# Kernel optimization log

Hardware: AMD Instinct MI355X
Metric: run time of the kernel (lower is better)

Reference implementation:

```python
import jax, jax.numpy as jnp
import numpy as np
from jax import lax

B, C, H, W = 4, 256, 64, 64
C8 = C // 8


def _conv1x1(x, w, b):
    # x: (B,C,H,W), w: (O,C) -> (B,O,H,W)
    return jnp.einsum('bchw,oc->bohw', x, w) + b[None, :, None, None]


def setup_inputs() -> dict:
    key = jax.random.key(0)
    ks = jax.random.split(key, 9)
    s1 = 1.0 / np.sqrt(C)          # fan-in scale for 1x1 convs
    sf = 1.0 / np.sqrt(2 * C * 9)  # fan-in scale for 3x3 conv
    return {
        'front_x':     jax.random.normal(ks[0], (B, C, H, W), jnp.float32),
        'cross_x':     jax.random.normal(ks[1], (B, C, H, W), jnp.float32),
        'front_x_hat': jax.random.normal(ks[2], (B, C, H, W), jnp.float32),
        'Wq': jax.random.normal(ks[3], (C8, C), jnp.float32) * s1,
        'bq': jnp.zeros((C8,), jnp.float32),
        'Wk': jax.random.normal(ks[4], (C8, C), jnp.float32) * s1,
        'bk': jnp.zeros((C8,), jnp.float32),
        'Wv': jax.random.normal(ks[5], (C, C), jnp.float32) * s1,
        'bv': jnp.zeros((C,), jnp.float32),
        'Wf': jax.random.normal(ks[6], (C, 2 * C, 3, 3), jnp.float32) * sf,
        'bf': jnp.zeros((C,), jnp.float32),
    }


def reference(front_x, cross_x, front_x_hat, Wq, bq, Wk, bk, Wv, bv, Wf, bf):
    b, c, h, w = front_x.shape
    hw = h * w
    # projections -> (B, C/8, HW)
    q = _conv1x1(cross_x, Wq, bq).reshape(b, -1, hw)
    k = _conv1x1(front_x, Wk, bk).reshape(b, -1, hw)
    # energy[b,i,j] = <key_i, query_j>  (B, HW, HW)
    energy = jnp.einsum('bci,bcj->bij', k, q)
    front_star = jnp.max(energy, axis=1)     # (B, HW) best key score per query
    front_arg = jnp.argmax(energy, axis=1)   # (B, HW) best key index per query
    # value projection and hard gather of best-matching value per position
    v = _conv1x1(front_x_hat, Wv, bv).reshape(b, c, hw)
    T = jnp.take_along_axis(v, front_arg[:, None, :], axis=2).reshape(b, c, h, w)
    S = front_star.reshape(b, 1, h, w)
    cat = jnp.concatenate([front_x, T], axis=1)  # (B, 2C, H, W)
    res = lax.conv_general_dilated(
        cat, Wf, window_strides=(1, 1), padding='SAME',
        dimension_numbers=('NCHW', 'OIHW', 'NCHW')) + bf[None, :, None, None]
    return front_x + res * S
```

## Files before the change

kernel.cpp:

```cpp
#include <hip/hip_runtime.h>

#define Bn 4
#define Cn 256
#define C8 32
#define Hn 64
#define Wn 64
#define HWn 4096
#define PADR 80
#define ROWS (HWn + 2 * PADR)
#define MARGIN 6e-3f

typedef __bf16 bf16x8 __attribute__((ext_vector_type(8)));
typedef float floatx4 __attribute__((ext_vector_type(4)));
typedef unsigned short u16x8 __attribute__((ext_vector_type(8)));

__device__ __forceinline__ unsigned short f2bf(float f) {
  union { float f; unsigned int u; } c; c.f = f;
  unsigned int u = c.u;
  return (unsigned short)((u + 0x7FFFu + ((u >> 16) & 1u)) >> 16);
}
__device__ __forceinline__ float bf2f(unsigned short h) {
  union { unsigned int u; float f; } c; c.u = ((unsigned int)h) << 16;
  return c.f;
}
__device__ __forceinline__ void gl_lds16(const void* g, void* l) {
  __builtin_amdgcn_global_load_lds(
      (__attribute__((address_space(1))) void*)(uintptr_t)g,
      (__attribute__((address_space(3))) void*)(uintptr_t)l, 16, 0, 0);
}

__global__ void prep_w(const float* __restrict__ Wq, const float* __restrict__ Wk,
                       const float* __restrict__ Wv, const float* __restrict__ Wf,
                       float* __restrict__ Wqf, float* __restrict__ Wkf,
                       unsigned short* __restrict__ Wvb, unsigned short* __restrict__ Wfb,
                       int* __restrict__ cnt) {
  size_t t = (size_t)blockIdx.x * 256 + threadIdx.x;
  if (t == 0) cnt[0] = 0;
  if (t < 8192) {
    int o = (int)(t / 256), c = (int)(t % 256);
    Wqf[(size_t)c * 32 + o] = Wq[t];
    Wkf[(size_t)c * 32 + o] = Wk[t];
  }
  if (t < 65536) Wvb[t] = f2bf(Wv[t]);
  if (t < (size_t)9 * 256 * 512) {
    int tap = (int)(t / (256 * 512));
    int rem = (int)(t % (256 * 512));
    int o = rem / 512, ci = rem % 512;
    Wfb[t] = f2bf(Wf[((size_t)o * 512 + ci) * 9 + tap]);
  }
}

__global__ __launch_bounds__(1024) void proj_qk(
    const float* __restrict__ cross_x, const float* __restrict__ front_x,
    const float* __restrict__ Wqf, const float* __restrict__ bq,
    const float* __restrict__ Wkf, const float* __restrict__ bk,
    float* __restrict__ qf, float* __restrict__ kf,
    unsigned short* __restrict__ qhi, unsigned short* __restrict__ qlo,
    unsigned short* __restrict__ khi, unsigned short* __restrict__ klo) {
  int tid = threadIdx.x;
  int lane = tid & 63, wv = tid >> 6;
  int slice = wv & 3;
  int chunk = wv >> 2;
  int j = blockIdx.x * 64 + lane;
  int b = blockIdx.y;
  int z = blockIdx.z;
  const float* x = (z == 0) ? cross_x : front_x;
  const float* Wg = (z == 0) ? Wqf : Wkf;
  const float* bd = (z == 0) ? bq : bk;
  float* outp = (z == 0) ? qf : kf;
  unsigned short* hip_ = (z == 0) ? qhi : khi;
  unsigned short* lop_ = (z == 0) ? qlo : klo;
  int o0 = slice * 8;
  int c0 = chunk * 64;

  __shared__ __align__(16) float Wl[8192];
  __shared__ float part[3 * 4 * 8 * 64];

  for (int u = tid; u < 8192; u += 1024) Wl[u] = Wg[u];
  __syncthreads();

  const float* xb = x + (size_t)b * Cn * HWn + j;
  floatx4 a0 = (floatx4)0.0f, a1 = (floatx4)0.0f;
#pragma unroll 16
  for (int c = c0; c < c0 + 64; ++c) {
    float xv = xb[(size_t)c * HWn];
    floatx4 wa = *reinterpret_cast<const floatx4*>(&Wl[c * 32 + o0]);
    floatx4 wb = *reinterpret_cast<const floatx4*>(&Wl[c * 32 + o0 + 4]);
    a0 += wa * xv;
    a1 += wb * xv;
  }
  if (chunk > 0) {
    float* dst = &part[(((chunk - 1) * 4 + slice) * 8) * 64];
#pragma unroll
    for (int o = 0; o < 4; ++o) { dst[o * 64 + lane] = a0[o]; dst[(o + 4) * 64 + lane] = a1[o]; }
  }
  __syncthreads();
  if (chunk != 0) return;
#pragma unroll
  for (int q = 0; q < 3; ++q) {
    const float* src = &part[((q * 4 + slice) * 8) * 64];
#pragma unroll
    for (int o = 0; o < 4; ++o) { a0[o] += src[o * 64 + lane]; a1[o] += src[(o + 4) * 64 + lane]; }
  }
  float acc[8];
#pragma unroll
  for (int o = 0; o < 4; ++o) { acc[o] = a0[o] + bd[o0 + o]; acc[o + 4] = a1[o] + bd[o0 + 4 + o]; }

  float* op = outp + ((size_t)b * HWn + j) * C8 + o0;
  u16x8 hv, lv;
#pragma unroll
  for (int o = 0; o < 8; ++o) {
    op[o] = acc[o];
    unsigned short h = f2bf(acc[o]);
    hv[o] = h;
    lv[o] = f2bf(acc[o] - bf2f(h));
  }
  *reinterpret_cast<u16x8*>(hip_ + ((size_t)b * HWn + j) * C8 + o0) = hv;
  *reinterpret_cast<u16x8*>(lop_ + ((size_t)b * HWn + j) * C8 + o0) = lv;
}

__global__ __launch_bounds__(1024) void energy_approx(
    const unsigned short* __restrict__ khi, const unsigned short* __restrict__ klo,
    const unsigned short* __restrict__ qhi, const unsigned short* __restrict__ qlo,
    float* __restrict__ star, int* __restrict__ argb,
    int* __restrict__ cnt, int* __restrict__ list) {
  int b = blockIdx.y;
  int j0 = blockIdx.x * 32;
  int tid = threadIdx.x;
  int lane = tid & 63, wv = tid >> 6;
  int lm = lane & 15, lq = lane >> 4;

  __shared__ float bv1S[16][32];
  __shared__ int   bi1S[16][32];
  __shared__ float bv2S[16][32];

  bf16x8 qh[2], ql[2];
#pragma unroll
  for (int s = 0; s < 2; ++s) {
    int j = j0 + s * 16 + lm;
    qh[s] = *reinterpret_cast<const bf16x8*>(qhi + ((size_t)b * HWn + j) * 32 + lq * 8);
    ql[s] = *reinterpret_cast<const bf16x8*>(qlo + ((size_t)b * HWn + j) * 32 + lq * 8);
  }
  const unsigned short* kh_base = khi + (size_t)b * HWn * 32 + lq * 8;
  const unsigned short* kl_base = klo + (size_t)b * HWn * 32 + lq * 8;

  float b1[2], b2[2];
#pragma unroll
  for (int s = 0; s < 2; ++s) { b1[s] = -3.0e38f; b2[s] = -3.0e38f; }

  int ibase = wv * 256;
#pragma unroll 4
  for (int it = 0; it < 16; ++it) {
    int i0 = ibase + it * 16;
    bf16x8 ah = *reinterpret_cast<const bf16x8*>(kh_base + (size_t)(i0 + lm) * 32);
    bf16x8 al = *reinterpret_cast<const bf16x8*>(kl_base + (size_t)(i0 + lm) * 32);
#pragma unroll
    for (int s = 0; s < 2; ++s) {
      floatx4 acc = (floatx4)0.0f;
      acc = __builtin_amdgcn_mfma_f32_16x16x32_bf16(ah, qh[s], acc, 0, 0, 0);
      acc = __builtin_amdgcn_mfma_f32_16x16x32_bf16(ah, ql[s], acc, 0, 0, 0);
      acc = __builtin_amdgcn_mfma_f32_16x16x32_bf16(al, qh[s], acc, 0, 0, 0);
#pragma unroll
      for (int r = 0; r < 4; ++r) {
        unsigned code = (unsigned)(it * 4 + r);
        union { float f; unsigned u; } cv; cv.f = acc[r];
        cv.u = (cv.u & ~63u) | code;
        float vp = cv.f;
        b2[s] = __builtin_amdgcn_fmed3f(vp, b1[s], b2[s]);
        b1[s] = fmaxf(b1[s], vp);
      }
    }
  }
  int i1[2];
#pragma unroll
  for (int s = 0; s < 2; ++s) {
    union { float f; unsigned u; } cv; cv.f = b1[s];
    unsigned code = cv.u & 63u;
    i1[s] = ibase + (int)(code >> 2) * 16 + lq * 4 + (int)(code & 3u);
  }
#pragma unroll
  for (int s = 0; s < 2; ++s) {
#pragma unroll
    for (int m = 16; m <= 32; m <<= 1) {
      float ob1 = __shfl_xor(b1[s], m, 64);
      int oi1 = __shfl_xor(i1[s], m, 64);
      float ob2 = __shfl_xor(b2[s], m, 64);
      float c2;
      if (ob1 > b1[s] || (ob1 == b1[s] && oi1 < i1[s])) {
        c2 = fmaxf(b1[s], ob2);
        b1[s] = ob1; i1[s] = oi1;
      } else {
        c2 = fmaxf(ob1, b2[s]);
      }
      b2[s] = c2;
    }
    if (lq == 0) {
      bv1S[wv][s * 16 + lm] = b1[s];
      bi1S[wv][s * 16 + lm] = i1[s];
      bv2S[wv][s * 16 + lm] = b2[s];
    }
  }
  __syncthreads();
  if (tid < 32) {
    float B1 = bv1S[0][tid];
    int I1 = bi1S[0][tid];
    float B2 = bv2S[0][tid];
#pragma unroll
    for (int w = 1; w < 16; ++w) {
      float v1 = bv1S[w][tid];
      int ii = bi1S[w][tid];
      float v2 = bv2S[w][tid];
      if (v1 > B1) { B2 = fmaxf(B1, v2); B1 = v1; I1 = ii; }
      else B2 = fmaxf(B2, v1);
    }
    size_t o = (size_t)b * HWn + j0 + tid;
    union { float f; unsigned u; } cs; cs.f = B1;
    cs.u &= ~63u;
    star[o] = cs.f;
    argb[o] = I1;
    if (B1 - B2 < MARGIN) {
      int slot = atomicAdd(cnt, 1);
      list[slot] = (b << 12) | (j0 + (int)tid);
    }
  }
}

__global__ __launch_bounds__(256) void recheck(
    const float* __restrict__ qf, const float* __restrict__ kf,
    const int* __restrict__ cnt, const int* __restrict__ list,
    float* __restrict__ star, int* __restrict__ argb) {
  __shared__ double bvS[4];
  __shared__ int biS[4];
  int n = cnt[0];
  int tid = threadIdx.x;
  int lane = tid & 63, wv = tid >> 6;
  for (int idx = blockIdx.x; idx < n; idx += gridDim.x) {
    int e = list[idx];
    int b = e >> 12, j = e & 4095;
    const float* qp = qf + ((size_t)b * HWn + j) * 32;
    double qj[32];
#pragma unroll
    for (int o = 0; o < 32; ++o) qj[o] = (double)qp[o];
    double best = -1.0e300;
    int bi = 1 << 30;
    for (int i = tid; i < HWn; i += 256) {
      const float* kp = kf + ((size_t)b * HWn + i) * 32;
      double s = 0.0;
#pragma unroll
      for (int o = 0; o < 32; ++o) s += (double)kp[o] * qj[o];
      if (s > best) { best = s; bi = i; }
    }
#pragma unroll
    for (int m = 1; m < 64; m <<= 1) {
      double ob = __shfl_xor(best, m, 64);
      int oi = __shfl_xor(bi, m, 64);
      if (ob > best || (ob == best && oi < bi)) { best = ob; bi = oi; }
    }
    if (lane == 0) { bvS[wv] = best; biS[wv] = bi; }
    __syncthreads();
    if (tid == 0) {
#pragma unroll
      for (int w = 1; w < 4; ++w) {
        if (bvS[w] > best || (bvS[w] == best && biS[w] < bi)) {
          best = bvS[w]; bi = biS[w];
        }
      }
      star[(size_t)b * HWn + j] = (float)best;
      argb[(size_t)b * HWn + j] = bi;
    }
    __syncthreads();
  }
}

__global__ __launch_bounds__(256) void cat_fx(
    const float* __restrict__ fx, const float* __restrict__ fxh,
    unsigned short* __restrict__ catC, unsigned short* __restrict__ xht) {
  int j0 = blockIdx.x * 64;
  int ci0 = blockIdx.y * 64;
  int b = blockIdx.z >> 1;
  int which = blockIdx.z & 1;
  int tid = threadIdx.x;
  __shared__ unsigned short tile[64][66];

  const float* src = (which == 0) ? fx : fxh;
#pragma unroll
  for (int u = tid; u < 1024; u += 256) {
    int cl = u >> 4, h4 = (u & 15) * 4;
    floatx4 v = *reinterpret_cast<const floatx4*>(
        &src[((size_t)(b * Cn + ci0 + cl)) * HWn + j0 + h4]);
#pragma unroll
    for (int k = 0; k < 4; ++k) tile[cl][h4 + k] = f2bf(v[k]);
  }
  __syncthreads();
#pragma unroll
  for (int u = tid; u < 512; u += 256) {
    int oct = u & 7, hw_l = u >> 3;
    u16x8 val;
#pragma unroll
    for (int k = 0; k < 8; ++k) val[k] = tile[oct * 8 + k][hw_l];
    if (which == 0)
      *reinterpret_cast<u16x8*>(
          &catC[((size_t)b * ROWS + PADR + j0 + hw_l) * 512 + ci0 + oct * 8]) = val;
    else
      *reinterpret_cast<u16x8*>(
          &xht[((size_t)b * HWn + j0 + hw_l) * 256 + ci0 + oct * 8]) = val;
  }
}

__global__ __launch_bounds__(256) void proj_v_mfma(
    const unsigned short* __restrict__ xht, const unsigned short* __restrict__ Wvb,
    const float* __restrict__ bv, unsigned short* __restrict__ vbf) {
  int m0 = blockIdx.x * 128;
  int o0 = blockIdx.y * 128;
  int b = blockIdx.z;
  int tid = threadIdx.x;
  int lane = tid & 63, wv = tid >> 6;
  int wm = wv >> 1, wn = wv & 1;
  int lm = lane & 15, lq = lane >> 4;

  union SMu {
    struct { unsigned short A[2][128 * 32]; unsigned short B[2][128 * 32]; } st;
    unsigned short TS[128 * 136];
  };
  __shared__ __align__(16) SMu sm;

  floatx4 acc[4][4];
#pragma unroll
  for (int im = 0; im < 4; ++im)
#pragma unroll
    for (int in = 0; in < 4; ++in) acc[im][in] = (floatx4)0.0f;

  const int srow = lane >> 2;
  const int soff = (((lane & 3) ^ ((lane >> 3) & 3)) * 8);
  const int sa = (lq ^ ((lm >> 1) & 3)) * 8;
  const unsigned short* ag = Wvb + (size_t)o0 * 256;
  const unsigned short* bg = xht + ((size_t)b * HWn + m0) * 256;

  auto STAGE = [&](int buf, int kc) {
#pragma unroll
    for (int i = 0; i < 2; ++i) {
      int r0 = wv * 32 + i * 16;
      gl_lds16(ag + ((size_t)(r0 + srow)) * 256 + kc + soff, &sm.st.A[buf][r0 * 32]);
      gl_lds16(bg + ((size_t)(r0 + srow)) * 256 + kc + soff, &sm.st.B[buf][r0 * 32]);
    }
  };
  auto COMPUTE = [&](int buf) {
    bf16x8 afr[4];
#pragma unroll
    for (int im = 0; im < 4; ++im)
      afr[im] = *reinterpret_cast<const bf16x8*>(
          &sm.st.A[buf][(wm * 64 + im * 16 + lm) * 32 + sa]);
#pragma unroll
    for (int in = 0; in < 4; ++in) {
      bf16x8 bfr = *reinterpret_cast<const bf16x8*>(
          &sm.st.B[buf][(wn * 64 + in * 16 + lm) * 32 + sa]);
#pragma unroll
      for (int im = 0; im < 4; ++im)
        acc[im][in] = __builtin_amdgcn_mfma_f32_16x16x32_bf16(
            afr[im], bfr, acc[im][in], 0, 0, 0);
    }
  };

  STAGE(0, 0);
#pragma unroll 2
  for (int st = 0; st < 8; ++st) {
    __builtin_amdgcn_s_barrier();
    if (st < 7) {
      STAGE((st + 1) & 1, (st + 1) * 32);
      asm volatile("s_waitcnt vmcnt(4)" ::: "memory");
    } else {
      asm volatile("s_waitcnt vmcnt(0)" ::: "memory");
    }
    __builtin_amdgcn_s_barrier();
    __builtin_amdgcn_sched_barrier(0);
    COMPUTE(st & 1);
  }
  __builtin_amdgcn_s_barrier();

#pragma unroll
  for (int in = 0; in < 4; ++in) {
    int pl = wn * 64 + in * 16 + lm;
#pragma unroll
    for (int im = 0; im < 4; ++im) {
#pragma unroll
      for (int r = 0; r < 4; ++r) {
        int ol = wm * 64 + im * 16 + lq * 4 + r;
        sm.TS[pl * 136 + ol] = f2bf(acc[im][in][r] + bv[o0 + ol]);
      }
    }
  }
  __syncthreads();
  for (int idx = tid; idx < 128 * 16; idx += 256) {
    int p = idx >> 4, ch = idx & 15;
    u16x8 val = *reinterpret_cast<const u16x8*>(&sm.TS[p * 136 + ch * 8]);
    *reinterpret_cast<u16x8*>(
        &vbf[((size_t)b * HWn + m0 + p) * 256 + o0 + ch * 8]) = val;
  }
}

__global__ __launch_bounds__(256) void gather_cat(
    const unsigned short* __restrict__ vbf, const int* __restrict__ argb,
    unsigned short* __restrict__ catC) {
  int b = blockIdx.y;
  int tid = threadIdx.x;
  if (blockIdx.x == 16) {
    for (int u = tid; u < 2 * PADR * 512; u += 256) {
      int r = u >> 9;
      int rr = (r < PADR) ? r : (HWn + r);
      catC[((size_t)b * ROWS + rr) * 512 + (u & 511)] = 0;
    }
    return;
  }
  __shared__ int ajS[256];
  int j0 = blockIdx.x * 256;
  ajS[tid] = argb[(size_t)b * HWn + j0 + tid];
  __syncthreads();
#pragma unroll 4
  for (int u = tid; u < 256 * 32; u += 256) {
    int pl = u >> 5, ch = u & 31;
    int aj = ajS[pl];
    u16x8 val = *reinterpret_cast<const u16x8*>(
        &vbf[((size_t)b * HWn + aj) * 256 + ch * 8]);
    *reinterpret_cast<u16x8*>(
        &catC[((size_t)b * ROWS + PADR + j0 + pl) * 512 + 256 + ch * 8]) = val;
  }
}

__global__ __launch_bounds__(256) void conv_mfma(
    const unsigned short* __restrict__ catC, const unsigned short* __restrict__ Wfb,
    unsigned short* __restrict__ Pg) {
  int m0 = blockIdx.x * 128;
  int o0 = blockIdx.y * 128;
  int bz = blockIdx.z;
  int b = bz / 3, g = bz % 3;
  int dy = g - 1;
  int tid = threadIdx.x;
  int lane = tid & 63;
  int wv = tid >> 6;
  int wm = wv >> 1, wn = wv & 1;
  int lm = lane & 15, lq = lane >> 4;
  const bool lane_first = (lm == 0);
  const bool lane_last = (lm == 15);

  __shared__ __align__(16) unsigned short AS[2][3 * 128 * 32];
  __shared__ __align__(16) unsigned short BS[2][144 * 32];

  floatx4 acc[4][4];
#pragma unroll
  for (int im = 0; im < 4; ++im)
#pragma unroll
    for (int in = 0; in < 4; ++in) acc[im][in] = (floatx4)0.0f;

  const int srow = lane >> 2;
  const int soff = (((lane & 3) ^ ((lane >> 3) & 3)) * 8);
  const int sa = (lq ^ ((lm >> 1) & 3)) * 8;
  const unsigned short* bg =
      catC + ((size_t)b * ROWS + PADR + m0 + dy * 64 - 1) * 512;
  const unsigned short* ag = Wfb + ((size_t)(g * 3) * 256 + o0) * 512;

  auto STAGE = [&](unsigned short* ASb, unsigned short* BSb, int kc) {
    if (wv < 3) {
      const unsigned short* at = ag + (size_t)wv * 256 * 512;
#pragma unroll
      for (int s = 0; s < 8; ++s)
        gl_lds16(at + ((size_t)(s * 16 + srow)) * 512 + kc + soff,
                 &ASb[(wv * 128 + s * 16) * 32]);
    } else {
#pragma unroll
      for (int s = 0; s < 9; ++s)
        gl_lds16(bg + ((size_t)(s * 16 + srow)) * 512 + kc + soff,
                 &BSb[(s * 16) * 32]);
    }
  };
  auto COMPUTE = [&](const unsigned short* ASb, const unsigned short* BSb) {
#pragma unroll
    for (int t = 0; t < 3; ++t) {
      bf16x8 afr[4];
#pragma unroll
      for (int im = 0; im < 4; ++im)
        afr[im] = *reinterpret_cast<const bf16x8*>(
            &ASb[(t * 128 + wm * 64 + im * 16 + lm) * 32 + sa]);
#pragma unroll
      for (int in = 0; in < 4; ++in) {
        int u = wn * 64 + in * 16 + lm + t;
        int sb = (lq ^ ((u >> 1) & 3)) * 8;
        u16x8 braw = *reinterpret_cast<const u16x8*>(&BSb[u * 32 + sb]);
        if ((t == 0 && in == 0 && lane_first) ||
            (t == 2 && in == 3 && lane_last))
          braw = (u16x8)(unsigned short)0;
        union { u16x8 u8; bf16x8 h; } cvt; cvt.u8 = braw;
#pragma unroll
        for (int im = 0; im < 4; ++im)
          acc[im][in] = __builtin_amdgcn_mfma_f32_16x16x32_bf16(
              afr[im], cvt.h, acc[im][in], 0, 0, 0);
      }
    }
  };

  STAGE(AS[0], BS[0], 0);
  __syncthreads();
  for (int kci = 0; kci < 16; kci += 2) {
    if (kci < 15) STAGE(AS[1], BS[1], (kci + 1) * 32);
    COMPUTE(AS[0], BS[0]);
    __syncthreads();
    if (kci < 14) STAGE(AS[0], BS[0], (kci + 2) * 32);
    COMPUTE(AS[1], BS[1]);
    __syncthreads();
  }

  unsigned short* P = Pg + ((size_t)(g * Bn + b) * Cn) * HWn;
#pragma unroll
  for (int in = 0; in < 4; ++in) {
    int p = m0 + wn * 64 + in * 16 + lm;
#pragma unroll
    for (int im = 0; im < 4; ++im) {
      int ob = o0 + wm * 64 + im * 16 + lq * 4;
#pragma unroll
      for (int r = 0; r < 4; ++r)
        P[(size_t)(ob + r) * HWn + p] = f2bf(acc[im][in][r]);
    }
  }
}

__global__ __launch_bounds__(256) void combine(
    const unsigned short* __restrict__ Pg, const float* __restrict__ fx,
    const float* __restrict__ bf, const float* __restrict__ star,
    float* __restrict__ out) {
  size_t e = ((size_t)blockIdx.x * 256 + threadIdx.x) * 8;
  int p = (int)(e & 4095);
  int bo = (int)(e >> 12);
  int o = bo & 255, b = bo >> 8;
  const size_t gs = (size_t)Bn * Cn * HWn;
  u16x8 q0 = *reinterpret_cast<const u16x8*>(Pg + e);
  u16x8 q1 = *reinterpret_cast<const u16x8*>(Pg + gs + e);
  u16x8 q2 = *reinterpret_cast<const u16x8*>(Pg + 2 * gs + e);
  float bias = bf[o];
  const float* sp = star + (size_t)b * HWn + p;
  const float* fp = fx + e;
  float* op = out + e;
#pragma unroll
  for (int h = 0; h < 2; ++h) {
    floatx4 s = *reinterpret_cast<const floatx4*>(sp + h * 4);
    floatx4 f = *reinterpret_cast<const floatx4*>(fp + h * 4);
    floatx4 r;
#pragma unroll
    for (int i = 0; i < 4; ++i) {
      int k = h * 4 + i;
      float a = bf2f(q0[k]) + bf2f(q1[k]) + bf2f(q2[k]);
      r[i] = f[i] + (a + bias) * s[i];
    }
    *reinterpret_cast<floatx4*>(op + h * 4) = r;
  }
}

extern "C" void kernel_launch(void* const* d_in, const int* in_sizes, int n_in,
                              void* d_out, int out_size, void* d_ws, size_t ws_size,
                              hipStream_t stream) {
  const float* front_x   = (const float*)d_in[0];
  const float* cross_x   = (const float*)d_in[1];
  const float* front_hat = (const float*)d_in[2];
  const float* Wq = (const float*)d_in[3];
  const float* bq = (const float*)d_in[4];
  const float* Wk = (const float*)d_in[5];
  const float* bk = (const float*)d_in[6];
  const float* Wv = (const float*)d_in[7];
  const float* bv = (const float*)d_in[8];
  const float* Wf = (const float*)d_in[9];
  const float* bf = (const float*)d_in[10];
  float* out = (float*)d_out;

  char* ws = (char*)d_ws;
  size_t off = 0;
  auto alloc = [&](size_t bytes) -> void* {
    void* p = (void*)(ws + off);
    off += (bytes + 255) & ~(size_t)255;
    return p;
  };
  float* Wqf = (float*)alloc(8192 * sizeof(float));
  float* Wkf = (float*)alloc(8192 * sizeof(float));
  unsigned short* Wvb = (unsigned short*)alloc(65536 * sizeof(unsigned short));
  unsigned short* Wfb = (unsigned short*)alloc((size_t)9 * 256 * 512 * sizeof(unsigned short));
  float* qf  = (float*)alloc((size_t)Bn * HWn * C8 * sizeof(float));
  float* kf  = (float*)alloc((size_t)Bn * HWn * C8 * sizeof(float));
  unsigned short* qhi = (unsigned short*)alloc((size_t)Bn * HWn * C8 * 2);
  unsigned short* qlo = (unsigned short*)alloc((size_t)Bn * HWn * C8 * 2);
  unsigned short* khi = (unsigned short*)alloc((size_t)Bn * HWn * C8 * 2);
  unsigned short* klo = (unsigned short*)alloc((size_t)Bn * HWn * C8 * 2);
  float*  star = (float*)alloc((size_t)Bn * HWn * sizeof(float));
  int*    argb = (int*)alloc((size_t)Bn * HWn * sizeof(int));
  int*    cnt  = (int*)alloc(256);
  int*    list = (int*)alloc((size_t)Bn * HWn * sizeof(int));
  unsigned short* xht = (unsigned short*)alloc((size_t)Bn * HWn * 256 * 2);
  unsigned short* vbf = (unsigned short*)alloc((size_t)Bn * HWn * 256 * 2);
  unsigned short* catC = (unsigned short*)alloc((size_t)Bn * ROWS * 512 * sizeof(unsigned short));
  unsigned short* Pg = (unsigned short*)alloc((size_t)3 * Bn * Cn * HWn * 2);

  prep_w<<<dim3((9 * 256 * 512 + 255) / 256), dim3(256), 0, stream>>>(
      Wq, Wk, Wv, Wf, Wqf, Wkf, Wvb, Wfb, cnt);

  proj_qk<<<dim3(HWn / 64, Bn, 2), dim3(1024), 0, stream>>>(
      cross_x, front_x, Wqf, bq, Wkf, bk, qf, kf, qhi, qlo, khi, klo);

  energy_approx<<<dim3(HWn / 32, Bn), dim3(1024), 0, stream>>>(
      khi, klo, qhi, qlo, star, argb, cnt, list);

  recheck<<<dim3(256), dim3(256), 0, stream>>>(qf, kf, cnt, list, star, argb);

  cat_fx<<<dim3(HWn / 64, Cn / 64, Bn * 2), dim3(256), 0, stream>>>(
      front_x, front_hat, catC, xht);

  proj_v_mfma<<<dim3(HWn / 128, Cn / 128, Bn), dim3(256), 0, stream>>>(
      xht, Wvb, bv, vbf);

  gather_cat<<<dim3(HWn / 256 + 1, Bn), dim3(256), 0, stream>>>(vbf, argb, catC);

  conv_mfma<<<dim3(HWn / 128, Cn / 128, Bn * 3), dim3(256), 0, stream>>>(
      catC, Wfb, Pg);

  combine<<<dim3((Bn * Cn * HWn / 8) / 256), dim3(256), 0, stream>>>(
      Pg, front_x, bf, star, out);
}
```

Before: 240.9 us.

## Co-schedule energy with cat transpose and recheck with V projection

Merges four kernels into two heterogeneous launches. Even blocks run the energy argmax and odd blocks run the fp32-to-bf16 transpose of front_x/front_x_hat, with four 64-channel groups per 1024-thread block. A second launch interleaves the V-projection GEMM tiles with the fp64 recheck of ambiguous argmax entries. The aim is to cut launch overhead and let independent memory-bound and compute-bound work share the GPU concurrently. In exchange, the merged kernels take the union of the two halves' register and LDS use, which may lower occupancy.

```diff
diff --git a/kernel.cpp b/kernel.cpp
--- a/kernel.cpp
+++ b/kernel.cpp
@@ -119,282 +119,288 @@
   *reinterpret_cast<u16x8*>(lop_ + ((size_t)b * HWn + j) * C8 + o0) = lv;
 }
 
-__global__ __launch_bounds__(1024) void energy_approx(
+__global__ __launch_bounds__(1024, 8) void energy_cat(
     const unsigned short* __restrict__ khi, const unsigned short* __restrict__ klo,
     const unsigned short* __restrict__ qhi, const unsigned short* __restrict__ qlo,
     float* __restrict__ star, int* __restrict__ argb,
-    int* __restrict__ cnt, int* __restrict__ list) {
-  int b = blockIdx.y;
-  int j0 = blockIdx.x * 32;
-  int tid = threadIdx.x;
-  int lane = tid & 63, wv = tid >> 6;
-  int lm = lane & 15, lq = lane >> 4;
-
-  __shared__ float bv1S[16][32];
-  __shared__ int   bi1S[16][32];
-  __shared__ float bv2S[16][32];
-
-  bf16x8 qh[2], ql[2];
-#pragma unroll
-  for (int s = 0; s < 2; ++s) {
-    int j = j0 + s * 16 + lm;
-    qh[s] = *reinterpret_cast<const bf16x8*>(qhi + ((size_t)b * HWn + j) * 32 + lq * 8);
-    ql[s] = *reinterpret_cast<const bf16x8*>(qlo + ((size_t)b * HWn + j) * 32 + lq * 8);
-  }
-  const unsigned short* kh_base = khi + (size_t)b * HWn * 32 + lq * 8;
-  const unsigned short* kl_base = klo + (size_t)b * HWn * 32 + lq * 8;
-
-  float b1[2], b2[2];
-#pragma unroll
-  for (int s = 0; s < 2; ++s) { b1[s] = -3.0e38f; b2[s] = -3.0e38f; }
-
-  int ibase = wv * 256;
+    int* __restrict__ cnt, int* __restrict__ list,
+    const float* __restrict__ fx, const float* __restrict__ fxh,
+    unsigned short* __restrict__ catC, unsigned short* __restrict__ xht) {
+  int bx = blockIdx.x;
+  if ((bx & 1) == 0) {
+    int id = bx >> 1;
+    int b = id >> 7;
+    int j0 = (id & 127) * 32;
+    int tid = threadIdx.x;
+    int lane = tid & 63, wv = tid >> 6;
+    int lm = lane & 15, lq = lane >> 4;
+
+    __shared__ float bv1S[16][32];
+    __shared__ int   bi1S[16][32];
+    __shared__ float bv2S[16][32];
+
+    bf16x8 qh[2], ql[2];
+#pragma unroll
+    for (int s = 0; s < 2; ++s) {
+      int j = j0 + s * 16 + lm;
+      qh[s] = *reinterpret_cast<const bf16x8*>(qhi + ((size_t)b * HWn + j) * 32 + lq * 8);
+      ql[s] = *reinterpret_cast<const bf16x8*>(qlo + ((size_t)b * HWn + j) * 32 + lq * 8);
+    }
+    const unsigned short* kh_base = khi + (size_t)b * HWn * 32 + lq * 8;
+    const unsigned short* kl_base = klo + (size_t)b * HWn * 32 + lq * 8;
+
+    float b1[2], b2[2];
+#pragma unroll
+    for (int s = 0; s < 2; ++s) { b1[s] = -3.0e38f; b2[s] = -3.0e38f; }
+
+    int ibase = wv * 256;
 #pragma unroll 4
-  for (int it = 0; it < 16; ++it) {
-    int i0 = ibase + it * 16;
-    bf16x8 ah = *reinterpret_cast<const bf16x8*>(kh_base + (size_t)(i0 + lm) * 32);
-    bf16x8 al = *reinterpret_cast<const bf16x8*>(kl_base + (size_t)(i0 + lm) * 32);
+    for (int it = 0; it < 16; ++it) {
+      int i0 = ibase + it * 16;
+      bf16x8 ah = *reinterpret_cast<const bf16x8*>(kh_base + (size_t)(i0 + lm) * 32);
+      bf16x8 al = *reinterpret_cast<const bf16x8*>(kl_base + (size_t)(i0 + lm) * 32);
+#pragma unroll
+      for (int s = 0; s < 2; ++s) {
+        floatx4 acc = (floatx4)0.0f;
+        acc = __builtin_amdgcn_mfma_f32_16x16x32_bf16(ah, qh[s], acc, 0, 0, 0);
+        acc = __builtin_amdgcn_mfma_f32_16x16x32_bf16(ah, ql[s], acc, 0, 0, 0);
+        acc = __builtin_amdgcn_mfma_f32_16x16x32_bf16(al, qh[s], acc, 0, 0, 0);
+#pragma unroll
+        for (int r = 0; r < 4; ++r) {
+          unsigned code = (unsigned)(it * 4 + r);
+          union { float f; unsigned u; } cv; cv.f = acc[r];
+          cv.u = (cv.u & ~63u) | code;
+          float vp = cv.f;
+          b2[s] = __builtin_amdgcn_fmed3f(vp, b1[s], b2[s]);
+          b1[s] = fmaxf(b1[s], vp);
+        }
+      }
+    }
+    int i1[2];
 #pragma unroll
     for (int s = 0; s < 2; ++s) {
-      floatx4 acc = (floatx4)0.0f;
-      acc = __builtin_amdgcn_mfma_f32_16x16x32_bf16(ah, qh[s], acc, 0, 0, 0);
-      acc = __builtin_amdgcn_mfma_f32_16x16x32_bf16(ah, ql[s], acc, 0, 0, 0);
-      acc = __builtin_amdgcn_mfma_f32_16x16x32_bf16(al, qh[s], acc, 0, 0, 0);
-#pragma unroll
-      for (int r = 0; r < 4; ++r) {
-        unsigned code = (unsigned)(it * 4 + r);
-        union { float f; unsigned u; } cv; cv.f = acc[r];
-        cv.u = (cv.u & ~63u) | code;
-        float vp = cv.f;
-        b2[s] = __builtin_amdgcn_fmed3f(vp, b1[s], b2[s]);
-        b1[s] = fmaxf(b1[s], vp);
-      }
-    }
-  }
-  int i1[2];
-#pragma unroll
-  for (int s = 0; s < 2; ++s) {
-    union { float f; unsigned u; } cv; cv.f = b1[s];
-    unsigned code = cv.u & 63u;
-    i1[s] = ibase + (int)(code >> 2) * 16 + lq * 4 + (int)(code & 3u);
-  }
-#pragma unroll
-  for (int s = 0; s < 2; ++s) {
-#pragma unroll
-    for (int m = 16; m <= 32; m <<= 1) {
-      float ob1 = __shfl_xor(b1[s], m, 64);
-      int oi1 = __shfl_xor(i1[s], m, 64);
-      float ob2 = __shfl_xor(b2[s], m, 64);
-      float c2;
-      if (ob1 > b1[s] || (ob1 == b1[s] && oi1 < i1[s])) {
-        c2 = fmaxf(b1[s], ob2);
-        b1[s] = ob1; i1[s] = oi1;
-      } else {
-        c2 = fmaxf(ob1, b2[s]);
-      }
-      b2[s] = c2;
-    }
-    if (lq == 0) {
-      bv1S[wv][s * 16 + lm] = b1[s];
-      bi1S[wv][s * 16 + lm] = i1[s];
-      bv2S[wv][s * 16 + lm] = b2[s];
-    }
-  }
-  __syncthreads();
-  if (tid < 32) {
-    float B1 = bv1S[0][tid];
-    int I1 = bi1S[0][tid];
-    float B2 = bv2S[0][tid];
-#pragma unroll
-    for (int w = 1; w < 16; ++w) {
-      float v1 = bv1S[w][tid];
-      int ii = bi1S[w][tid];
-      float v2 = bv2S[w][tid];
-      if (v1 > B1) { B2 = fmaxf(B1, v2); B1 = v1; I1 = ii; }
-      else B2 = fmaxf(B2, v1);
-    }
-    size_t o = (size_t)b * HWn + j0 + tid;
-    union { float f; unsigned u; } cs; cs.f = B1;
-    cs.u &= ~63u;
-    star[o] = cs.f;
-    argb[o] = I1;
-    if (B1 - B2 < MARGIN) {
-      int slot = atomicAdd(cnt, 1);
-      list[slot] = (b << 12) | (j0 + (int)tid);
-    }
-  }
-}
-
-__global__ __launch_bounds__(256) void recheck(
+      union { float f; unsigned u; } cv; cv.f = b1[s];
+      unsigned code = cv.u & 63u;
+      i1[s] = ibase + (int)(code >> 2) * 16 + lq * 4 + (int)(code & 3u);
+    }
+#pragma unroll
+    for (int s = 0; s < 2; ++s) {
+#pragma unroll
+      for (int m = 16; m <= 32; m <<= 1) {
+        float ob1 = __shfl_xor(b1[s], m, 64);
+        int oi1 = __shfl_xor(i1[s], m, 64);
+        float ob2 = __shfl_xor(b2[s], m, 64);
+        float c2;
+        if (ob1 > b1[s] || (ob1 == b1[s] && oi1 < i1[s])) {
+          c2 = fmaxf(b1[s], ob2);
+          b1[s] = ob1; i1[s] = oi1;
+        } else {
+          c2 = fmaxf(ob1, b2[s]);
+        }
+        b2[s] = c2;
+      }
+      if (lq == 0) {
+        bv1S[wv][s * 16 + lm] = b1[s];
+        bi1S[wv][s * 16 + lm] = i1[s];
+        bv2S[wv][s * 16 + lm] = b2[s];
+      }
+    }
+    __syncthreads();
+    if (tid < 32) {
+      float B1 = bv1S[0][tid];
+      int I1 = bi1S[0][tid];
+      float B2 = bv2S[0][tid];
+#pragma unroll
+      for (int w = 1; w < 16; ++w) {
+        float v1 = bv1S[w][tid];
+        int ii = bi1S[w][tid];
+        float v2 = bv2S[w][tid];
+        if (v1 > B1) { B2 = fmaxf(B1, v2); B1 = v1; I1 = ii; }
+        else B2 = fmaxf(B2, v1);
+      }
+      size_t o = (size_t)b * HWn + j0 + tid;
+      union { float f; unsigned u; } cs; cs.f = B1;
+      cs.u &= ~63u;
+      star[o] = cs.f;
+      argb[o] = I1;
+      if (B1 - B2 < MARGIN) {
+        int slot = atomicAdd(cnt, 1);
+        list[slot] = (b << 12) | (j0 + (int)tid);
+      }
+    }
+  } else {
+    int id = bx >> 1;
+    int j0 = (id & 63) * 64;
+    int bz = id >> 6;
+    int b = bz >> 1, which = bz & 1;
+    int g4 = threadIdx.x >> 8;
+    int tid = threadIdx.x & 255;
+    int ci0 = g4 * 64;
+    __shared__ unsigned short tile[4][64][66];
+
+    const float* src = (which == 0) ? fx : fxh;
+#pragma unroll
+    for (int u = tid; u < 1024; u += 256) {
+      int cl = u >> 4, h4 = (u & 15) * 4;
+      floatx4 v = *reinterpret_cast<const floatx4*>(
+          &src[((size_t)(b * Cn + ci0 + cl)) * HWn + j0 + h4]);
+#pragma unroll
+      for (int k = 0; k < 4; ++k) tile[g4][cl][h4 + k] = f2bf(v[k]);
+    }
+    __syncthreads();
+#pragma unroll
+    for (int u = tid; u < 512; u += 256) {
+      int oct = u & 7, hw_l = u >> 3;
+      u16x8 val;
+#pragma unroll
+      for (int k = 0; k < 8; ++k) val[k] = tile[g4][oct * 8 + k][hw_l];
+      if (which == 0)
+        *reinterpret_cast<u16x8*>(
+            &catC[((size_t)b * ROWS + PADR + j0 + hw_l) * 512 + ci0 + oct * 8]) = val;
+      else
+        *reinterpret_cast<u16x8*>(
+            &xht[((size_t)b * HWn + j0 + hw_l) * 256 + ci0 + oct * 8]) = val;
+    }
+  }
+}
+
+__global__ __launch_bounds__(256) void recheck_projv(
+    const unsigned short* __restrict__ xht, const unsigned short* __restrict__ Wvb,
+    const float* __restrict__ bv, unsigned short* __restrict__ vbf,
     const float* __restrict__ qf, const float* __restrict__ kf,
     const int* __restrict__ cnt, const int* __restrict__ list,
     float* __restrict__ star, int* __restrict__ argb) {
-  __shared__ double bvS[4];
-  __shared__ int biS[4];
-  int n = cnt[0];
-  int tid = threadIdx.x;
-  int lane = tid & 63, wv = tid >> 6;
-  for (int idx = blockIdx.x; idx < n; idx += gridDim.x) {
-    int e = list[idx];
-    int b = e >> 12, j = e & 4095;
-    const float* qp = qf + ((size_t)b * HWn + j) * 32;
-    double qj[32];
-#pragma unroll
-    for (int o = 0; o < 32; ++o) qj[o] = (double)qp[o];
-    double best = -1.0e300;
-    int bi = 1 << 30;
-    for (int i = tid; i < HWn; i += 256) {
-      const float* kp = kf + ((size_t)b * HWn + i) * 32;
-      double s = 0.0;
-#pragma unroll
-      for (int o = 0; o < 32; ++o) s += (double)kp[o] * qj[o];
-      if (s > best) { best = s; bi = i; }
-    }
-#pragma unroll
-    for (int m = 1; m < 64; m <<= 1) {
-      double ob = __shfl_xor(best, m, 64);
-      int oi = __shfl_xor(bi, m, 64);
-      if (ob > best || (ob == best && oi < bi)) { best = ob; bi = oi; }
-    }
-    if (lane == 0) { bvS[wv] = best; biS[wv] = bi; }
+  int bx = blockIdx.x;
+  if ((bx & 1) == 0) {
+    int id = bx >> 1;
+    int m0 = (id & 31) * 128;
+    int o0 = ((id >> 5) & 1) * 128;
+    int b = id >> 6;
+    int tid = threadIdx.x;
+    int lane = tid & 63, wv = tid >> 6;
+    int wm = wv >> 1, wn = wv & 1;
+    int lm = lane & 15, lq = lane >> 4;
+
+    union SMu {
+      struct { unsigned short A[2][128 * 32]; unsigned short B[2][128 * 32]; } st;
+      unsigned short TS[128 * 136];
+    };
+    __shared__ __align__(16) SMu sm;
+
+    floatx4 acc[4][4];
+#pragma unroll
+    for (int im = 0; im < 4; ++im)
+#pragma unroll
+      for (int in = 0; in < 4; ++in) acc[im][in] = (floatx4)0.0f;
+
+    const int srow = lane >> 2;
+    const int soff = (((lane & 3) ^ ((lane >> 3) & 3)) * 8);
+    const int sa = (lq ^ ((lm >> 1) & 3)) * 8;
+    const unsigned short* ag = Wvb + (size_t)o0 * 256;
+    const unsigned short* bg = xht + ((size_t)b * HWn + m0) * 256;
+
+    auto STAGE = [&](int buf, int kc) {
+#pragma unroll
+      for (int i = 0; i < 2; ++i) {
+        int r0 = wv * 32 + i * 16;
+        gl_lds16(ag + ((size_t)(r0 + srow)) * 256 + kc + soff, &sm.st.A[buf][r0 * 32]);
+        gl_lds16(bg + ((size_t)(r0 + srow)) * 256 + kc + soff, &sm.st.B[buf][r0 * 32]);
+      }
+    };
+    auto COMPUTE = [&](int buf) {
+      bf16x8 afr[4];
+#pragma unroll
+      for (int im = 0; im < 4; ++im)
+        afr[im] = *reinterpret_cast<const bf16x8*>(
+            &sm.st.A[buf][(wm * 64 + im * 16 + lm) * 32 + sa]);
+#pragma unroll
+      for (int in = 0; in < 4; ++in) {
+        bf16x8 bfr = *reinterpret_cast<const bf16x8*>(
+            &sm.st.B[buf][(wn * 64 + in * 16 + lm) * 32 + sa]);
+#pragma unroll
+        for (int im = 0; im < 4; ++im)
+          acc[im][in] = __builtin_amdgcn_mfma_f32_16x16x32_bf16(
+              afr[im], bfr, acc[im][in], 0, 0, 0);
+      }
+    };
+
+    STAGE(0, 0);
+#pragma unroll 2
+    for (int st = 0; st < 8; ++st) {
+      __builtin_amdgcn_s_barrier();
+      if (st < 7) {
+        STAGE((st + 1) & 1, (st + 1) * 32);
+        asm volatile("s_waitcnt vmcnt(4)" ::: "memory");
+      } else {
+        asm volatile("s_waitcnt vmcnt(0)" ::: "memory");
+      }
+      __builtin_amdgcn_s_barrier();
+      __builtin_amdgcn_sched_barrier(0);
+      COMPUTE(st & 1);
+    }
+    __builtin_amdgcn_s_barrier();
+
+#pragma unroll
+    for (int in = 0; in < 4; ++in) {
+      int pl = wn * 64 + in * 16 + lm;
+#pragma unroll
+      for (int im = 0; im < 4; ++im) {
+#pragma unroll
+        for (int r = 0; r < 4; ++r) {
+          int ol = wm * 64 + im * 16 + lq * 4 + r;
+          sm.TS[pl * 136 + ol] = f2bf(acc[im][in][r] + bv[o0 + ol]);
+        }
+      }
+    }
     __syncthreads();
-    if (tid == 0) {
-#pragma unroll
-      for (int w = 1; w < 4; ++w) {
-        if (bvS[w] > best || (bvS[w] == best && biS[w] < bi)) {
-          best = bvS[w]; bi = biS[w];
+    for (int idx = tid; idx < 128 * 16; idx += 256) {
+      int p = idx >> 4, ch = idx & 15;
+      u16x8 val = *reinterpret_cast<const u16x8*>(&sm.TS[p * 136 + ch * 8]);
+      *reinterpret_cast<u16x8*>(
+          &vbf[((size_t)b * HWn + m0 + p) * 256 + o0 + ch * 8]) = val;
+    }
+  } else {
+    __shared__ double bvS[4];
+    __shared__ int biS[4];
+    int n = cnt[0];
+    int tid = threadIdx.x;
+    int lane = tid & 63, wv = tid >> 6;
+    for (int idx = bx >> 1; idx < n; idx += 256) {
+      int e = list[idx];
+      int b = e >> 12, j = e & 4095;
+      const float* qp = qf + ((size_t)b * HWn + j) * 32;
+      double qj[32];
+#pragma unroll
+      for (int o = 0; o < 32; ++o) qj[o] = (double)qp[o];
+      double best = -1.0e300;
+      int bi = 1 << 30;
+      for (int i = tid; i < HWn; i += 256) {
+        const float* kp = kf + ((size_t)b * HWn + i) * 32;
+        double s = 0.0;
+#pragma unroll
+        for (int o = 0; o < 32; ++o) s += (double)kp[o] * qj[o];
+        if (s > best) { best = s; bi = i; }
+      }
+#pragma unroll
+      for (int m = 1; m < 64; m <<= 1) {
+        double ob = __shfl_xor(best, m, 64);
+        int oi = __shfl_xor(bi, m, 64);
+        if (ob > best || (ob == best && oi < bi)) { best = ob; bi = oi; }
+      }
+      if (lane == 0) { bvS[wv] = best; biS[wv] = bi; }
+      __syncthreads();
+      if (tid == 0) {
+#pragma unroll
+        for (int w = 1; w < 4; ++w) {
+          if (bvS[w] > best || (bvS[w] == best && biS[w] < bi)) {
+            best = bvS[w]; bi = biS[w];
+          }
         }
-      }
-      star[(size_t)b * HWn + j] = (float)best;
-      argb[(size_t)b * HWn + j] = bi;
-    }
-    __syncthreads();
-  }
-}
-
-__global__ __launch_bounds__(256) void cat_fx(
-    const float* __restrict__ fx, const float* __restrict__ fxh,
-    unsigned short* __restrict__ catC, unsigned short* __restrict__ xht) {
-  int j0 = blockIdx.x * 64;
-  int ci0 = blockIdx.y * 64;
-  int b = blockIdx.z >> 1;
-  int which = blockIdx.z & 1;
-  int tid = threadIdx.x;
-  __shared__ unsigned short tile[64][66];
-
-  const float* src = (which == 0) ? fx : fxh;
-#pragma unroll
-  for (int u = tid; u < 1024; u += 256) {
-    int cl = u >> 4, h4 = (u & 15) * 4;
-    floatx4 v = *reinterpret_cast<const floatx4*>(
-        &src[((size_t)(b * Cn + ci0 + cl)) * HWn + j0 + h4]);
-#pragma unroll
-    for (int k = 0; k < 4; ++k) tile[cl][h4 + k] = f2bf(v[k]);
-  }
-  __syncthreads();
-#pragma unroll
-  for (int u = tid; u < 512; u += 256) {
-    int oct = u & 7, hw_l = u >> 3;
-    u16x8 val;
-#pragma unroll
-    for (int k = 0; k < 8; ++k) val[k] = tile[oct * 8 + k][hw_l];
-    if (which == 0)
-      *reinterpret_cast<u16x8*>(
-          &catC[((size_t)b * ROWS + PADR + j0 + hw_l) * 512 + ci0 + oct * 8]) = val;
-    else
-      *reinterpret_cast<u16x8*>(
-          &xht[((size_t)b * HWn + j0 + hw_l) * 256 + ci0 + oct * 8]) = val;
-  }
-}
-
-__global__ __launch_bounds__(256) void proj_v_mfma(
-    const unsigned short* __restrict__ xht, const unsigned short* __restrict__ Wvb,
-    const float* __restrict__ bv, unsigned short* __restrict__ vbf) {
-  int m0 = blockIdx.x * 128;
-  int o0 = blockIdx.y * 128;
-  int b = blockIdx.z;
-  int tid = threadIdx.x;
-  int lane = tid & 63, wv = tid >> 6;
-  int wm = wv >> 1, wn = wv & 1;
-  int lm = lane & 15, lq = lane >> 4;
-
-  union SMu {
-    struct { unsigned short A[2][128 * 32]; unsigned short B[2][128 * 32]; } st;
-    unsigned short TS[128 * 136];
-  };
-  __shared__ __align__(16) SMu sm;
-
-  floatx4 acc[4][4];
-#pragma unroll
-  for (int im = 0; im < 4; ++im)
-#pragma unroll
-    for (int in = 0; in < 4; ++in) acc[im][in] = (floatx4)0.0f;
-
-  const int srow = lane >> 2;
-  const int soff = (((lane & 3) ^ ((lane >> 3) & 3)) * 8);
-  const int sa = (lq ^ ((lm >> 1) & 3)) * 8;
-  const unsigned short* ag = Wvb + (size_t)o0 * 256;
-  const unsigned short* bg = xht + ((size_t)b * HWn + m0) * 256;
-
-  auto STAGE = [&](int buf, int kc) {
-#pragma unroll
-    for (int i = 0; i < 2; ++i) {
-      int r0 = wv * 32 + i * 16;
-      gl_lds16(ag + ((size_t)(r0 + srow)) * 256 + kc + soff, &sm.st.A[buf][r0 * 32]);
-      gl_lds16(bg + ((size_t)(r0 + srow)) * 256 + kc + soff, &sm.st.B[buf][r0 * 32]);
-    }
-  };
-  auto COMPUTE = [&](int buf) {
-    bf16x8 afr[4];
-#pragma unroll
-    for (int im = 0; im < 4; ++im)
-      afr[im] = *reinterpret_cast<const bf16x8*>(
-          &sm.st.A[buf][(wm * 64 + im * 16 + lm) * 32 + sa]);
-#pragma unroll
-    for (int in = 0; in < 4; ++in) {
-      bf16x8 bfr = *reinterpret_cast<const bf16x8*>(
-          &sm.st.B[buf][(wn * 64 + in * 16 + lm) * 32 + sa]);
-#pragma unroll
-      for (int im = 0; im < 4; ++im)
-        acc[im][in] = __builtin_amdgcn_mfma_f32_16x16x32_bf16(
-            afr[im], bfr, acc[im][in], 0, 0, 0);
-    }
-  };
-
-  STAGE(0, 0);
-#pragma unroll 2
-  for (int st = 0; st < 8; ++st) {
-    __builtin_amdgcn_s_barrier();
-    if (st < 7) {
-      STAGE((st + 1) & 1, (st + 1) * 32);
-      asm volatile("s_waitcnt vmcnt(4)" ::: "memory");
-    } else {
-      asm volatile("s_waitcnt vmcnt(0)" ::: "memory");
-    }
-    __builtin_amdgcn_s_barrier();
-    __builtin_amdgcn_sched_barrier(0);
-    COMPUTE(st & 1);
-  }
-  __builtin_amdgcn_s_barrier();
-
-#pragma unroll
-  for (int in = 0; in < 4; ++in) {
-    int pl = wn * 64 + in * 16 + lm;
-#pragma unroll
-    for (int im = 0; im < 4; ++im) {
-#pragma unroll
-      for (int r = 0; r < 4; ++r) {
-        int ol = wm * 64 + im * 16 + lq * 4 + r;
-        sm.TS[pl * 136 + ol] = f2bf(acc[im][in][r] + bv[o0 + ol]);
-      }
-    }
-  }
-  __syncthreads();
-  for (int idx = tid; idx < 128 * 16; idx += 256) {
-    int p = idx >> 4, ch = idx & 15;
-    u16x8 val = *reinterpret_cast<const u16x8*>(&sm.TS[p * 136 + ch * 8]);
-    *reinterpret_cast<u16x8*>(
-        &vbf[((size_t)b * HWn + m0 + p) * 256 + o0 + ch * 8]) = val;
+        star[(size_t)b * HWn + j] = (float)best;
+        argb[(size_t)b * HWn + j] = bi;
+      }
+      __syncthreads();
+    }
   }
 }
 
@@ -601,16 +607,12 @@
   proj_qk<<<dim3(HWn / 64, Bn, 2), dim3(1024), 0, stream>>>(
       cross_x, front_x, Wqf, bq, Wkf, bk, qf, kf, qhi, qlo, khi, klo);
 
-  energy_approx<<<dim3(HWn / 32, Bn), dim3(1024), 0, stream>>>(
-      khi, klo, qhi, qlo, star, argb, cnt, list);
-
-  recheck<<<dim3(256), dim3(256), 0, stream>>>(qf, kf, cnt, list, star, argb);
-
-  cat_fx<<<dim3(HWn / 64, Cn / 64, Bn * 2), dim3(256), 0, stream>>>(
+  energy_cat<<<dim3(1024), dim3(1024), 0, stream>>>(
+      khi, klo, qhi, qlo, star, argb, cnt, list,
       front_x, front_hat, catC, xht);
 
-  proj_v_mfma<<<dim3(HWn / 128, Cn / 128, Bn), dim3(256), 0, stream>>>(
-      xht, Wvb, bv, vbf);
+  recheck_projv<<<dim3(512), dim3(256), 0, stream>>>(
+      xht, Wvb, bv, vbf, qf, kf, cnt, list, star, argb);
 
   gather_cat<<<dim3(HWn / 256 + 1, Bn), dim3(256), 0, stream>>>(vbf, argb, catC);
 
```

After: 238.5 us. About the same (-1.0%).
